# Optimization experiments

Measured on AMD Instinct MI355X. Metric: run time of the kernel, lower is better.

The kernel has to match this reference:

```python
import jax, jax.numpy as jnp
from jax import lax
import numpy as np

# Module config (kornia ConvSoftArgmax3d defaults)
KD, KH, KW = 3, 3, 3
STRIDE = (1, 1, 1)
PAD = (1, 1, 1)
TEMPERATURE = 1.0
EPS = 1e-8

SHAPE = (4, 8, 16, 256, 256)  # (B, C, D, H, W)


def _window_grid_kernel3d(kd, kh, kw):
    # kornia._get_window_grid_kernel3d: (3, 1, kd, kh, kw), channels = [z, x, y],
    # each axis normalized to [-1, 1] over the window.
    z = jnp.linspace(-1.0, 1.0, kd) if kd > 1 else jnp.zeros((1,))
    x = jnp.linspace(-1.0, 1.0, kw) if kw > 1 else jnp.zeros((1,))
    y = jnp.linspace(-1.0, 1.0, kh) if kh > 1 else jnp.zeros((1,))
    Z = jnp.broadcast_to(z[:, None, None], (kd, kh, kw))
    X = jnp.broadcast_to(x[None, None, :], (kd, kh, kw))
    Y = jnp.broadcast_to(y[None, :, None], (kd, kh, kw))
    return jnp.stack([Z, X, Y])[:, None].astype(jnp.float32)


def _center_kernel3d(kd, kh, kw):
    # kornia._get_center_kernel3d: diagonal (3, 3, kd, kh, kw) kernel picking the
    # window-center coordinate (average of 2 middle pixels for even sizes).
    def rng(n):
        return (n // 2, n // 2 + 1) if n % 2 != 0 else (n // 2 - 1, n // 2 + 1)
    (d1, d2), (h1, h2), (w1, w2) = rng(kd), rng(kh), rng(kw)
    num = float((d2 - d1) * (h2 - h1) * (w2 - w1))
    k = np.zeros((3, 3, kd, kh, kw), np.float32)
    for i in range(3):
        k[i, i, d1:d2, h1:h2, w1:w2] = 1.0 / num
    return jnp.asarray(k)


def _global_grid(D, H, W):
    # kornia.create_meshgrid3d(..., normalized=False).permute(0,4,1,2,3):
    # shape (1, 3, D, H, W), channels = [z, x, y] in pixel coordinates.
    z = jnp.arange(D, dtype=jnp.float32)
    y = jnp.arange(H, dtype=jnp.float32)
    x = jnp.arange(W, dtype=jnp.float32)
    Z = jnp.broadcast_to(z[:, None, None], (D, H, W))
    X = jnp.broadcast_to(x[None, None, :], (D, H, W))
    Y = jnp.broadcast_to(y[None, :, None], (D, H, W))
    return jnp.stack([Z, X, Y])[None]


def _forward(x):
    B, C, D, H, W = x.shape
    xi = x.reshape(B * C, 1, D, H, W)

    # exp-normalize trick; global max is detached in kornia
    x_max = lax.stop_gradient(jnp.max(xi, axis=(2, 3, 4), keepdims=True))
    x_exp = jnp.exp((xi - x_max) / TEMPERATURE)

    win = (1, 1, KD, KH, KW)
    strides = (1, 1) + STRIDE
    pool_pads = [(0, 0), (0, 0)] + [(p, p) for p in PAD]
    # pool_coef * avg_pool3d (count_include_pad=True) == zero-padded sum pool
    def sum_pool(v):
        return lax.reduce_window(v, 0.0, lax.add, win, strides, pool_pads)

    den = sum_pool(x_exp) + EPS  # (B*C, 1, Do, Ho, Wo)

    dn = ('NCDHW', 'OIDHW', 'NCDHW')
    conv_pad = [(p, p) for p in PAD]

    # soft-argmax relative coordinates within each window
    coords = lax.conv_general_dilated(
        x_exp, _window_grid_kernel3d(KD, KH, KW), STRIDE, conv_pad,
        dimension_numbers=dn)
    coords = coords / den

    # add global window-center coordinates
    grid_pooled = lax.conv_general_dilated(
        _global_grid(D, H, W), _center_kernel3d(KD, KH, KW), STRIDE, conv_pad,
        dimension_numbers=dn)
    coords = coords + grid_pooled

    Do, Ho, Wo = coords.shape[2], coords.shape[3], coords.shape[4]
    coords = coords.reshape(B, C, 3, Do, Ho, Wo)

    # soft-pooled response value (output_value=True, strict_maxima_bonus=0)
    vals = (sum_pool(x_exp * xi) / den).reshape(B, C, Do, Ho, Wo)
    return coords, vals


def setup_inputs() -> dict:
    key = jax.random.key(0)
    x = jax.random.normal(key, SHAPE, dtype=jnp.float32)
    return {"x": x}


def reference(x):
    return _forward(x)
```

## Files before the change

kernel.cpp:

```cpp
#include <hip/hip_runtime.h>
#include <math.h>

#define BC 32
#define DD 16
#define HH 256
#define WW 256
#define PLANE (HH * WW)
#define CH_ELEMS (DD * PLANE)
#define COORD_ELEMS (BC * 3 * CH_ELEMS)
#define TS 68

typedef float vf4 __attribute__((ext_vector_type(4)));

__global__ __launch_bounds__(256) void chmax_part(const float* __restrict__ x,
                                                  float* __restrict__ part) {
    const int ch = blockIdx.y;
    const int tid = threadIdx.x;
    const float4* p4 = (const float4*)(x + (size_t)ch * CH_ELEMS) + (size_t)blockIdx.x * 4096;
    float m = -3.402823466e38f;
#pragma unroll
    for (int i = 0; i < 16; ++i) {
        float4 v = p4[tid + i * 256];
        m = fmaxf(m, fmaxf(fmaxf(v.x, v.y), fmaxf(v.z, v.w)));
    }
#pragma unroll
    for (int off = 32; off > 0; off >>= 1)
        m = fmaxf(m, __shfl_down(m, off, 64));
    __shared__ float sm[4];
    if ((tid & 63) == 0) sm[tid >> 6] = m;
    __syncthreads();
    if (tid == 0)
        part[ch * 64 + blockIdx.x] = fmaxf(fmaxf(sm[0], sm[1]), fmaxf(sm[2], sm[3]));
}

__global__ __launch_bounds__(64) void chmax_final(const float* __restrict__ part,
                                                  float* __restrict__ mx) {
    const int ch = blockIdx.x, tid = threadIdx.x;
    float m = part[ch * 64 + tid];
#pragma unroll
    for (int off = 32; off > 0; off >>= 1)
        m = fmaxf(m, __shfl_down(m, off, 64));
    if (tid == 0) mx[ch] = m;
}

__global__ __launch_bounds__(256) void csam3d_main(const float* __restrict__ xin_all,
                                                   const float* __restrict__ mx,
                                                   float* __restrict__ out) {
    const int ch = blockIdx.z;
    const int h0 = blockIdx.y * 16;
    const int w0 = blockIdx.x * 64;
    const int tid = threadIdx.x;
    const float cmax = mx[ch];
    const float* __restrict__ xin = xin_all + (size_t)ch * CH_ELEMS;

    float* __restrict__ outz = out + (size_t)(ch * 3 + 0) * CH_ELEMS;
    float* __restrict__ outx = out + (size_t)(ch * 3 + 1) * CH_ELEMS;
    float* __restrict__ outy = out + (size_t)(ch * 3 + 2) * CH_ELEMS;
    float* __restrict__ outv = out + COORD_ELEMS + (size_t)ch * CH_ELEMS;

    __shared__ __align__(16) float eS[2][18 * TS];
    __shared__ __align__(16) float vS[2][18 * TS];

    const int hl = tid >> 4;
    const int wb = (tid & 15) << 2;

    float s2[3][4], mx2[3][4], my2[3][4], sv2[3][4];

#define STAGE(I) do {                                                         \
    const int din_ = (I) - 1;                                                 \
    float* eb_ = eS[(I) & 1];                                                 \
    float* vb_ = vS[(I) & 1];                                                 \
    if (din_ < 0 || din_ >= DD) {                                             \
        for (int s5 = tid; s5 < 18 * TS; s5 += 256) { eb_[s5] = 0.f; vb_[s5] = 0.f; } \
    } else {                                                                  \
        const float* xp_ = xin + (size_t)din_ * PLANE;                        \
        _Pragma("unroll")                                                     \
        for (int it = 0; it < 5; ++it) {                                      \
            int s5 = tid + it * 256;                                          \
            if (s5 < 18 * 66) {                                               \
                int lh = s5 / 66;                                             \
                int lw = s5 - lh * 66;                                        \
                int gh = h0 + lh - 1;                                         \
                int gw = w0 + lw - 1;                                         \
                float ev = 0.f, vv = 0.f;                                     \
                if ((unsigned)gh < (unsigned)HH && (unsigned)gw < (unsigned)WW) { \
                    float xv = xp_[gh * WW + gw];                             \
                    ev = __expf(xv - cmax);                                   \
                    vv = ev * xv;                                             \
                }                                                             \
                eb_[lh * TS + lw] = ev;                                       \
                vb_[lh * TS + lw] = vv;                                       \
            }                                                                 \
        }                                                                     \
    }                                                                         \
} while (0)

#define LDROW(PTR) do {                                                       \
    float4 a_ = *(const float4*)(PTR);                                        \
    float2 b_ = *(const float2*)((PTR) + 4);                                  \
    v0 = a_.x; v1 = a_.y; v2 = a_.z; v3 = a_.w; v4 = b_.x; v5 = b_.y;         \
} while (0)

#define CSLICE(I, SC) do {                                                    \
    const float* eb_ = eS[(I) & 1] + hl * TS + wb;                            \
    const float* vb_ = vS[(I) & 1] + hl * TS + wb;                            \
    float v0, v1, v2, v3, v4, v5;                                             \
    LDROW(eb_);                                                               \
    float c0 = v0, c1 = v1, c2 = v2, c3 = v3, c4 = v4, c5 = v5;               \
    float d0 = -v0, d1 = -v1, d2 = -v2, d3 = -v3, d4 = -v4, d5 = -v5;         \
    LDROW(eb_ + TS);                                                          \
    c0 += v0; c1 += v1; c2 += v2; c3 += v3; c4 += v4; c5 += v5;               \
    LDROW(eb_ + 2 * TS);                                                      \
    c0 += v0; c1 += v1; c2 += v2; c3 += v3; c4 += v4; c5 += v5;               \
    d0 += v0; d1 += v1; d2 += v2; d3 += v3; d4 += v4; d5 += v5;               \
    LDROW(vb_);                                                               \
    float g0 = v0, g1 = v1, g2 = v2, g3 = v3, g4 = v4, g5 = v5;               \
    LDROW(vb_ + TS);                                                          \
    g0 += v0; g1 += v1; g2 += v2; g3 += v3; g4 += v4; g5 += v5;               \
    LDROW(vb_ + 2 * TS);                                                      \
    g0 += v0; g1 += v1; g2 += v2; g3 += v3; g4 += v4; g5 += v5;               \
    s2[SC][0] = c0 + c1 + c2;  s2[SC][1] = c1 + c2 + c3;                      \
    s2[SC][2] = c2 + c3 + c4;  s2[SC][3] = c3 + c4 + c5;                      \
    mx2[SC][0] = c2 - c0; mx2[SC][1] = c3 - c1;                               \
    mx2[SC][2] = c4 - c2; mx2[SC][3] = c5 - c3;                               \
    my2[SC][0] = d0 + d1 + d2;  my2[SC][1] = d1 + d2 + d3;                    \
    my2[SC][2] = d2 + d3 + d4;  my2[SC][3] = d3 + d4 + d5;                    \
    sv2[SC][0] = g0 + g1 + g2;  sv2[SC][1] = g1 + g2 + g3;                    \
    sv2[SC][2] = g2 + g3 + g4;  sv2[SC][3] = g3 + g4 + g5;                    \
} while (0)

#define EMIT(I, SA, SB, SC) do {                                              \
    const int dout_ = (I) - 2;                                                \
    vf4 oz, ox, oy, ov;                                                       \
    _Pragma("unroll")                                                         \
    for (int k = 0; k < 4; ++k) {                                             \
        float S  = s2[SA][k] + s2[SB][k] + s2[SC][k];                         \
        float Mz = s2[SC][k] - s2[SA][k];                                     \
        float Mx = mx2[SA][k] + mx2[SB][k] + mx2[SC][k];                      \
        float My = my2[SA][k] + my2[SB][k] + my2[SC][k];                      \
        float Sv = sv2[SA][k] + sv2[SB][k] + sv2[SC][k];                      \
        float inv = __builtin_amdgcn_rcpf(S + 1e-8f);                         \
        oz[k] = Mz * inv + (float)dout_;                                      \
        ox[k] = Mx * inv + (float)(w0 + wb + k);                              \
        oy[k] = My * inv + (float)(h0 + hl);                                  \
        ov[k] = Sv * inv;                                                     \
    }                                                                         \
    size_t off_ = (size_t)dout_ * PLANE + (size_t)(h0 + hl) * WW + (w0 + wb); \
    __builtin_nontemporal_store(oz, (vf4*)(outz + off_));                     \
    __builtin_nontemporal_store(ox, (vf4*)(outx + off_));                     \
    __builtin_nontemporal_store(oy, (vf4*)(outy + off_));                     \
    __builtin_nontemporal_store(ov, (vf4*)(outv + off_));                     \
} while (0)

#define STEP(I, SC, SA, SB) do {                                              \
    STAGE(I);                                                                 \
    __syncthreads();                                                          \
    CSLICE(I, SC);                                                            \
    if ((I) >= 2) EMIT(I, SA, SB, SC);                                        \
} while (0)

    for (int ii = 0; ii < 18; ii += 3) {
        STEP(ii + 0, 0, 1, 2);
        STEP(ii + 1, 1, 2, 0);
        STEP(ii + 2, 2, 0, 1);
    }
}

extern "C" void kernel_launch(void* const* d_in, const int* in_sizes, int n_in,
                              void* d_out, int out_size, void* d_ws, size_t ws_size,
                              hipStream_t stream) {
    const float* x = (const float*)d_in[0];
    float* out = (float*)d_out;
    float* part = (float*)d_ws;
    float* mx = part + 2048;

    chmax_part<<<dim3(64, 32), 256, 0, stream>>>(x, part);
    chmax_final<<<32, 64, 0, stream>>>(part, mx);
    csam3d_main<<<dim3(4, 16, 32), 256, 0, stream>>>(x, mx, out);
}
```

Before: 633.3 us.

## Software-pipeline depth-slice loads with register prefetch two slices ahead

Index and bounds math for the halo tile load is precomputed once per thread. Each depth slice is fetched into registers two iterations ahead, then written to the other LDS buffer while the current slice is computed, so one barrier per step covers both the write and the compute. The aim is to hide global load latency behind the convolution math and drop the repeated per-slice address computation. In exchange it uses more registers for the prefetch buffers and fully unrolls the 18 steps, which may lower occupancy.

```diff
diff --git a/kernel.cpp b/kernel.cpp
--- a/kernel.cpp
+++ b/kernel.cpp
@@ -64,33 +64,42 @@
     const int hl = tid >> 4;
     const int wb = (tid & 15) << 2;
 
+    int soff[5];
+    int slds[5];
+    bool sval[5];
+#pragma unroll
+    for (int it = 0; it < 5; ++it) {
+        int s5 = tid + it * 256;
+        int lh = s5 / 66;
+        int lw = s5 - lh * 66;
+        int gh = h0 + lh - 1;
+        int gw = w0 + lw - 1;
+        bool v = (s5 < 18 * 66) && ((unsigned)gh < (unsigned)HH) && ((unsigned)gw < (unsigned)WW);
+        sval[it] = v;
+        soff[it] = v ? (gh * WW + gw) : 0;
+        slds[it] = lh * TS + lw;
+    }
+
+    float pfA[5], pfB[5];
+
     float s2[3][4], mx2[3][4], my2[3][4], sv2[3][4];
 
-#define STAGE(I) do {                                                         \
-    const int din_ = (I) - 1;                                                 \
-    float* eb_ = eS[(I) & 1];                                                 \
-    float* vb_ = vS[(I) & 1];                                                 \
-    if (din_ < 0 || din_ >= DD) {                                             \
-        for (int s5 = tid; s5 < 18 * TS; s5 += 256) { eb_[s5] = 0.f; vb_[s5] = 0.f; } \
-    } else {                                                                  \
-        const float* xp_ = xin + (size_t)din_ * PLANE;                        \
-        _Pragma("unroll")                                                     \
-        for (int it = 0; it < 5; ++it) {                                      \
-            int s5 = tid + it * 256;                                          \
-            if (s5 < 18 * 66) {                                               \
-                int lh = s5 / 66;                                             \
-                int lw = s5 - lh * 66;                                        \
-                int gh = h0 + lh - 1;                                         \
-                int gw = w0 + lw - 1;                                         \
-                float ev = 0.f, vv = 0.f;                                     \
-                if ((unsigned)gh < (unsigned)HH && (unsigned)gw < (unsigned)WW) { \
-                    float xv = xp_[gh * WW + gw];                             \
-                    ev = __expf(xv - cmax);                                   \
-                    vv = ev * xv;                                             \
-                }                                                             \
-                eb_[lh * TS + lw] = ev;                                       \
-                vb_[lh * TS + lw] = vv;                                       \
-            }                                                                 \
+#define PREFETCH(DIN, PF) do {                                                \
+    const float* xp_ = xin + (size_t)(DIN) * PLANE;                           \
+    _Pragma("unroll")                                                         \
+    for (int it = 0; it < 5; ++it) PF[it] = xp_[soff[it]];                    \
+} while (0)
+
+#define WRITESLICE(BUF, PF, ZERO) do {                                        \
+    float* eb_ = eS[BUF];                                                     \
+    float* vb_ = vS[BUF];                                                     \
+    _Pragma("unroll")                                                         \
+    for (int it = 0; it < 5; ++it) {                                          \
+        if (it < 4 || tid < 18 * 66 - 1024) {   \
+            float xv_ = PF[it];                                               \
+            float ev_ = (sval[it] && !(ZERO)) ? __expf(xv_ - cmax) : 0.f;     \
+            eb_[slds[it]] = ev_;                                              \
+            vb_[slds[it]] = ev_ * xv_;                                        \
         }                                                                     \
     }                                                                         \
 } while (0)
@@ -152,18 +161,40 @@
     __builtin_nontemporal_store(ov, (vf4*)(outv + off_));                     \
 } while (0)
 
-#define STEP(I, SC, SA, SB) do {                                              \
-    STAGE(I);                                                                 \
-    __syncthreads();                                                          \
+#define STEP(I, SC, SA, SB, PF) do {                                          \
+    if ((I) < 17) WRITESLICE((I + 1) & 1, PF, (I) >= 16);                     \
+    if ((I) <= 13) PREFETCH((I) + 2, PF);    \
     CSLICE(I, SC);                                                            \
     if ((I) >= 2) EMIT(I, SA, SB, SC);                                        \
-} while (0)
-
-    for (int ii = 0; ii < 18; ii += 3) {
-        STEP(ii + 0, 0, 1, 2);
-        STEP(ii + 1, 1, 2, 0);
-        STEP(ii + 2, 2, 0, 1);
+    __syncthreads();                                                          \
+} while (0)
+
+    PREFETCH(0, pfA);
+    PREFETCH(1, pfB);
+    for (int i = tid; i < 18 * TS; i += 256) {
+        eS[0][i] = 0.f;
+        vS[0][i] = 0.f;
     }
+    __syncthreads();
+
+    STEP(0,  0, 1, 2, pfA);
+    STEP(1,  1, 2, 0, pfB);
+    STEP(2,  2, 0, 1, pfA);
+    STEP(3,  0, 1, 2, pfB);
+    STEP(4,  1, 2, 0, pfA);
+    STEP(5,  2, 0, 1, pfB);
+    STEP(6,  0, 1, 2, pfA);
+    STEP(7,  1, 2, 0, pfB);
+    STEP(8,  2, 0, 1, pfA);
+    STEP(9,  0, 1, 2, pfB);
+    STEP(10, 1, 2, 0, pfA);
+    STEP(11, 2, 0, 1, pfB);
+    STEP(12, 0, 1, 2, pfA);
+    STEP(13, 1, 2, 0, pfB);
+    STEP(14, 2, 0, 1, pfA);
+    STEP(15, 0, 1, 2, pfB);
+    STEP(16, 1, 2, 0, pfA);
+    STEP(17, 2, 0, 1, pfB);
 }
 
 extern "C" void kernel_launch(void* const* d_in, const int* in_sizes, int n_in,
```

After: 632.5 us. Within noise of the previous version (-0.1%).
